# Kernel tuning notes

Hardware: AMD Instinct MI355X
Metric: run time of the kernel (lower is better)

## Reference

```python
import jax, jax.numpy as jnp
import numpy as np

B, H, L, D, BLK = 2, 16, 2048, 64, 32
NB = L // BLK          # 64 blocks per side
WINDOW = 8             # causal local window, in blocks


def make_layout():
    # [H, NB, NB] int32: block (i, j) active iff 0 <= i - j < WINDOW (causal local band)
    bi = jnp.arange(NB)
    band = ((bi[:, None] - bi[None, :]) >= 0) & ((bi[:, None] - bi[None, :]) < WINDOW)
    return jnp.broadcast_to(band[None].astype(jnp.int32), (H, NB, NB))


def setup_inputs() -> dict:
    rng = jax.random.key(0)
    kq, kk, kv, kp = jax.random.split(rng, 4)
    return {
        "query": jax.random.normal(kq, (B, H, L, D), dtype=jnp.float32),
        "key": jax.random.normal(kk, (B, H, L, D), dtype=jnp.float32),
        "value": jax.random.normal(kv, (B, H, L, D), dtype=jnp.float32),
        "key_padding_mask": jax.random.normal(kp, (B, L), dtype=jnp.float32),
        "layout": make_layout(),
    }


def reference(query, key, value, key_padding_mask, layout):
    # query/key/value: [B, H, L, D]; layout: [H, NB, NB] block sparsity pattern
    bsz, num_heads, tgt_len, head_dim = query.shape
    blk = tgt_len // layout.shape[1]
    scaling = float(head_dim) ** (-0.5)

    # SDD: scores only on active blocks. Reference computes dense then masks
    # inactive blocks to -inf, matching blocksparse softmax semantics exactly.
    scores = jnp.einsum("bhqd,bhkd->bhqk", query, key) * scaling
    # key_padding_mask_mode='add': added to logits, broadcast over queries
    scores = scores + key_padding_mask[:, None, None, :]

    # expand block layout [H, NB, NB] -> element mask [H, L, L]
    block_mask = jnp.repeat(jnp.repeat(layout.astype(bool), blk, axis=1), blk, axis=2)
    scores = jnp.where(block_mask[None], scores, -jnp.inf)

    probs = jax.nn.softmax(scores, axis=-1)  # zeros outside active blocks
    # DSD: probs @ value
    attn_output = jnp.einsum("bhqk,bhkd->bhqd", probs, value)
    return attn_output
```

## Files before the change

### kernel.cpp

```cpp
#include <hip/hip_runtime.h>

#define B_   2
#define H_   16
#define L_   2048
#define D_   64
#define BLK_ 32
#define NB_  64

#define KSW 64
#define VS  40
#define OS  65

typedef __bf16 bf16x8 __attribute__((ext_vector_type(8)));
typedef float  f32x4  __attribute__((ext_vector_type(4)));
typedef unsigned short u16x8 __attribute__((ext_vector_type(8)));

__device__ inline unsigned short f2bf(float f) {
    unsigned int u = __builtin_bit_cast(unsigned int, f);
    unsigned int r = u + 0x7fffu + ((u >> 16) & 1u);
    return (unsigned short)(r >> 16);
}
#define WG_BARRIER() asm volatile("s_waitcnt lgkmcnt(0)\n\ts_barrier" ::: "memory")

__global__ __launch_bounds__(128)
__attribute__((amdgpu_waves_per_eu(4, 4)))
void sparse_attn_kernel(const float* __restrict__ qg,
                        const float* __restrict__ kg,
                        const float* __restrict__ vg,
                        const float* __restrict__ kpm,
                        const int*   __restrict__ layout,
                        float* __restrict__ outg)
{
    __shared__ __align__(16) union {
        struct {
            unsigned short Ks[2][BLK_ * KSW];
            unsigned short Vt[2][D_ * VS];
        } s;
        float Os[32 * OS];
    } Lds;

    const int tid  = threadIdx.x;
    const int wave = tid >> 6;
    const int lane = tid & 63;
    const int quad = lane >> 4;
    const int l15  = lane & 15;

    const int phys = blockIdx.x;
    const int lw   = (phys & 7) * 256 + (phys >> 3);
    const int i = lw & 63;
    const int h = (lw >> 6) & 15;
    const int b = lw >> 10;

    const size_t bh = (size_t)(b * H_ + h);
    const float* kbase = kg + bh * L_ * D_;
    const float* vbase = vg + bh * L_ * D_;
    const float* kpp   = kpm + (size_t)b * L_;
    const int*   layrow = layout + (h * NB_ + i) * NB_;

    const int jbeg = i - 7;
    int act[8];
    #pragma unroll
    for (int s = 0; s < 8; ++s) {
        const int j = jbeg + s;
        act[s] = (j >= 0) ? layrow[j] : 0;
    }

    bf16x8 aq[2];
    {
        const float* qrow = qg + (bh * L_ + (size_t)i * BLK_ + wave * 16 + l15) * D_;
        #pragma unroll
        for (int ks = 0; ks < 2; ++ks) {
            float4 x = *(const float4*)&qrow[ks * 32 + quad * 8];
            float4 y = *(const float4*)&qrow[ks * 32 + quad * 8 + 4];
            u16x8 pk;
            pk[0]=f2bf(x.x); pk[1]=f2bf(x.y); pk[2]=f2bf(x.z); pk[3]=f2bf(x.w);
            pk[4]=f2bf(y.x); pk[5]=f2bf(y.y); pk[6]=f2bf(y.z); pk[7]=f2bf(y.w);
            aq[ks] = __builtin_bit_cast(bf16x8, pk);
        }
    }

    auto clampj = [&](int j) { return j < 0 ? 0 : j; };

    u16x8 kc[2][2];
    u16x8 vc[2][2];

    auto loadT = [&](int jc, int slot) {
        const float* kb = kbase + (size_t)jc * BLK_ * D_;
        float4 a0 = *(const float4*)&kb[tid * 8];
        float4 a1 = *(const float4*)&kb[tid * 8 + 4];
        float4 b0 = *(const float4*)&kb[(tid + 128) * 8];
        float4 b1 = *(const float4*)&kb[(tid + 128) * 8 + 4];
        u16x8 k0, k1;
        k0[0]=f2bf(a0.x); k0[1]=f2bf(a0.y); k0[2]=f2bf(a0.z); k0[3]=f2bf(a0.w);
        k0[4]=f2bf(a1.x); k0[5]=f2bf(a1.y); k0[6]=f2bf(a1.z); k0[7]=f2bf(a1.w);
        k1[0]=f2bf(b0.x); k1[1]=f2bf(b0.y); k1[2]=f2bf(b0.z); k1[3]=f2bf(b0.w);
        k1[4]=f2bf(b1.x); k1[5]=f2bf(b1.y); k1[6]=f2bf(b1.z); k1[7]=f2bf(b1.w);
        kc[slot][0] = k0; kc[slot][1] = k1;
        const float* vb = vbase + (size_t)jc * BLK_ * D_;
        #pragma unroll
        for (int cc = 0; cc < 2; ++cc) {
            u16x8 pv;
            #pragma unroll
            for (int r = 0; r < 4; ++r) {
                pv[r]     = f2bf(vb[(wave * 8 + cc * 4 + r) * D_ + lane]);
                pv[4 + r] = f2bf(vb[(16 + wave * 8 + cc * 4 + r) * D_ + lane]);
            }
            vc[slot][cc] = pv;
        }
    };

    auto storeT = [&](int buf, int slot) {
        const int row = tid >> 3, oct = tid & 7;
        *(u16x8*)&Lds.s.Ks[buf][row * KSW + ((oct ^ (row & 7)) * 8)]        = kc[slot][0];
        *(u16x8*)&Lds.s.Ks[buf][(16 + row) * KSW + ((oct ^ (row & 7)) * 8)] = kc[slot][1];
        const int swz = lane & 3;
        #pragma unroll
        for (int cc = 0; cc < 2; ++cc)
            *(u16x8*)&Lds.s.Vt[buf][lane * VS + (((2 * wave + cc) ^ swz) * 8)] = vc[slot][cc];
    };

    float lsum = 0.f;
    f32x4 Ot[4];
    #pragma unroll
    for (int t = 0; t < 4; ++t) Ot[t] = (f32x4){0.f, 0.f, 0.f, 0.f};

    auto computeT = [&](int buf, int j) {
        float4 kp0 = *(const float4*)&kpp[j * BLK_ + quad * 4];
        float4 kp1 = *(const float4*)&kpp[j * BLK_ + 16 + quad * 4];
        f32x4 st0 = {0.f,0.f,0.f,0.f}, st1 = {0.f,0.f,0.f,0.f};
        #pragma unroll
        for (int ks = 0; ks < 2; ++ks) {
            const int co = (((ks * 4 + quad) ^ (l15 & 7)) * 8);
            bf16x8 ka  = *(const bf16x8*)&Lds.s.Ks[buf][l15 * KSW + co];
            bf16x8 kb2 = *(const bf16x8*)&Lds.s.Ks[buf][(16 + l15) * KSW + co];
            st0 = __builtin_amdgcn_mfma_f32_16x16x32_bf16(ka,  aq[ks], st0, 0, 0, 0);
            st1 = __builtin_amdgcn_mfma_f32_16x16x32_bf16(kb2, aq[ks], st1, 0, 0, 0);
        }
        u16x8 bpk;
        #pragma unroll
        for (int r = 0; r < 4; ++r) {
            float p0 = __expf(st0[r] * 0.125f + kp0[r]);
            float p1 = __expf(st1[r] * 0.125f + kp1[r]);
            lsum += p0 + p1;
            bpk[r]     = f2bf(p0);
            bpk[4 + r] = f2bf(p1);
        }
        bf16x8 bp = __builtin_bit_cast(bf16x8, bpk);
        const int swzv = l15 & 3;
        #pragma unroll
        for (int t = 0; t < 4; ++t) {
            bf16x8 av = *(const bf16x8*)&Lds.s.Vt[buf][(t * 16 + l15) * VS + ((quad ^ swzv) * 8)];
            Ot[t] = __builtin_amdgcn_mfma_f32_16x16x32_bf16(av, bp, Ot[t], 0, 0, 0);
        }
    };

    loadT(clampj(jbeg), 0);
    storeT(0, 0);
    loadT(clampj(jbeg + 1), 1);
    WG_BARRIER();

    int cur = 0;
    #pragma unroll
    for (int s = 0; s < 8; ++s) {
        const int j = jbeg + s;
        if (s <= 5) loadT(clampj(j + 2), s & 1);
        if (act[s] != 0) computeT(cur, j);
        if (s < 7) storeT(cur ^ 1, (s + 1) & 1);
        WG_BARRIER();
        cur ^= 1;
    }

    lsum += __shfl_xor(lsum, 16);
    lsum += __shfl_xor(lsum, 32);
    const float rinv = 1.0f / lsum;

    float* osw = &Lds.Os[(wave * 16) * OS];
    #pragma unroll
    for (int t = 0; t < 4; ++t)
        #pragma unroll
        for (int r = 0; r < 4; ++r)
            osw[l15 * OS + t * 16 + quad * 4 + r] = Ot[t][r] * rinv;
    asm volatile("s_waitcnt lgkmcnt(0)" ::: "memory");

    const int qrow = lane >> 2, sc = lane & 3;
    float* outp = outg + (bh * L_ + (size_t)i * BLK_ + wave * 16) * D_;
    #pragma unroll
    for (int c = 0; c < 4; ++c) {
        float4 gv;
        #pragma unroll
        for (int r = 0; r < 4; ++r) gv[r] = osw[qrow * OS + c * 16 + sc * 4 + r];
        *(float4*)&outp[qrow * D_ + c * 16 + sc * 4] = gv;
    }
}

extern "C" void kernel_launch(void* const* d_in, const int* in_sizes, int n_in,
                              void* d_out, int out_size, void* d_ws, size_t ws_size,
                              hipStream_t stream) {
    const float* q      = (const float*)d_in[0];
    const float* k      = (const float*)d_in[1];
    const float* v      = (const float*)d_in[2];
    const float* kpmask = (const float*)d_in[3];
    const int*   layout = (const int*)d_in[4];
    float* out = (float*)d_out;

    dim3 grid(B_ * H_ * NB_);
    dim3 block(128);
    sparse_attn_kernel<<<grid, block, 0, stream>>>(q, k, v, kpmask, layout, out);
}
```

Before: 106.3 us.

## Precompute bf16 K and transposed V in a prep kernel, drop LDS staging

Adds a prep kernel that converts K to bf16 and V to a transposed bf16 layout in workspace once. The attention kernel then runs one wave per 16 query rows, loading MFMA operands straight from global memory with no LDS buffers or barriers, and writes the output directly from registers. This removes the eight-fold redundant fp32 loading and conversion of each K/V block across neighbouring query blocks and all barrier synchronisation. In exchange it adds a second launch, a workspace round trip, and global loads issued on the critical path without double-buffering.

```diff
diff --git a/kernel.cpp b/kernel.cpp
--- a/kernel.cpp
+++ b/kernel.cpp
@@ -6,10 +6,7 @@
 #define D_   64
 #define BLK_ 32
 #define NB_  64
-
-#define KSW 64
-#define VS  40
-#define OS  65
+#define BH_  (B_ * H_)
 
 typedef __bf16 bf16x8 __attribute__((ext_vector_type(8)));
 typedef float  f32x4  __attribute__((ext_vector_type(4)));
@@ -20,176 +17,144 @@
     unsigned int r = u + 0x7fffu + ((u >> 16) & 1u);
     return (unsigned short)(r >> 16);
 }
-#define WG_BARRIER() asm volatile("s_waitcnt lgkmcnt(0)\n\ts_barrier" ::: "memory")
+__device__ inline unsigned int pkt(float lo, float hi) {
+    return __builtin_amdgcn_perm(__builtin_bit_cast(unsigned int, hi),
+                                 __builtin_bit_cast(unsigned int, lo), 0x07060302u);
+}
 
-__global__ __launch_bounds__(128)
+__global__ __launch_bounds__(64)
+void prep_kernel(const float* __restrict__ kg, const float* __restrict__ vg,
+                 unsigned short* __restrict__ kbo, unsigned short* __restrict__ vto)
+{
+    const int lane = threadIdx.x;
+    const int wg = blockIdx.x;
+    const int j  = wg & (NB_ - 1);
+    const int bh = wg >> 6;
+
+    const float* ks = kg + ((size_t)bh * L_ + (size_t)j * BLK_) * D_;
+    unsigned short* kd = kbo + ((size_t)bh * L_ + (size_t)j * BLK_) * D_;
+    #pragma unroll
+    for (int e = 0; e < 4; ++e) {
+        float4 x = *(const float4*)&ks[lane * 32 + e * 8];
+        float4 y = *(const float4*)&ks[lane * 32 + e * 8 + 4];
+        u16x8 w;
+        w[0]=f2bf(x.x); w[1]=f2bf(x.y); w[2]=f2bf(x.z); w[3]=f2bf(x.w);
+        w[4]=f2bf(y.x); w[5]=f2bf(y.y); w[6]=f2bf(y.z); w[7]=f2bf(y.w);
+        *(u16x8*)&kd[lane * 32 + e * 8] = w;
+    }
+
+    const float* vs = vg + ((size_t)bh * L_ + (size_t)j * BLK_) * D_;
+    unsigned short* vd = vto + ((size_t)bh * D_ + lane) * L_ + (size_t)j * BLK_;
+    #pragma unroll
+    for (int e = 0; e < 4; ++e) {
+        u16x8 w;
+        #pragma unroll
+        for (int q = 0; q < 8; ++q) {
+            const int key = (q >> 2) * 16 + e * 4 + (q & 3);
+            w[q] = f2bf(vs[key * D_ + lane]);
+        }
+        *(u16x8*)&vd[e * 8] = w;
+    }
+}
+
+__global__ __launch_bounds__(64)
 __attribute__((amdgpu_waves_per_eu(4, 4)))
-void sparse_attn_kernel(const float* __restrict__ qg,
-                        const float* __restrict__ kg,
-                        const float* __restrict__ vg,
-                        const float* __restrict__ kpm,
-                        const int*   __restrict__ layout,
-                        float* __restrict__ outg)
+void attn_kernel(const float* __restrict__ qg,
+                 const float* __restrict__ kpm,
+                 const int*   __restrict__ layout,
+                 const unsigned short* __restrict__ kbi,
+                 const unsigned short* __restrict__ vti,
+                 float* __restrict__ outg)
 {
-    __shared__ __align__(16) union {
-        struct {
-            unsigned short Ks[2][BLK_ * KSW];
-            unsigned short Vt[2][D_ * VS];
-        } s;
-        float Os[32 * OS];
-    } Lds;
-
-    const int tid  = threadIdx.x;
-    const int wave = tid >> 6;
-    const int lane = tid & 63;
-    const int quad = lane >> 4;
-    const int l15  = lane & 15;
+    const int lane = threadIdx.x & 63;
+    const int quad = lane >> 4, l15 = lane & 15;
 
     const int phys = blockIdx.x;
-    const int lw   = (phys & 7) * 256 + (phys >> 3);
-    const int i = lw & 63;
-    const int h = (lw >> 6) & 15;
-    const int b = lw >> 10;
+    const int lw = (phys & 7) * 512 + (phys >> 3);
+    const int hf = lw & 1;
+    const int i  = (lw >> 1) & 63;
+    const int bh = lw >> 7;
+    const int b = bh >> 4, h = bh & 15;
 
-    const size_t bh = (size_t)(b * H_ + h);
-    const float* kbase = kg + bh * L_ * D_;
-    const float* vbase = vg + bh * L_ * D_;
-    const float* kpp   = kpm + (size_t)b * L_;
-    const int*   layrow = layout + (h * NB_ + i) * NB_;
+    const unsigned short* kbb = kbi + (size_t)bh * L_ * D_;
+    const unsigned short* vtb = vti + (size_t)bh * D_ * L_;
+    const float* kpp = kpm + (size_t)b * L_;
+    const int* layrow = layout + (h * NB_ + i) * NB_;
 
     const int jbeg = i - 7;
     int act[8];
     #pragma unroll
-    for (int s = 0; s < 8; ++s) {
-        const int j = jbeg + s;
-        act[s] = (j >= 0) ? layrow[j] : 0;
-    }
+    for (int s = 0; s < 8; ++s) { const int j = jbeg + s; act[s] = (j >= 0) ? layrow[j] : 0; }
 
     bf16x8 aq[2];
     {
-        const float* qrow = qg + (bh * L_ + (size_t)i * BLK_ + wave * 16 + l15) * D_;
+        const float* qrow = qg + ((size_t)bh * L_ + (size_t)i * BLK_ + hf * 16 + l15) * D_;
         #pragma unroll
         for (int ks = 0; ks < 2; ++ks) {
             float4 x = *(const float4*)&qrow[ks * 32 + quad * 8];
             float4 y = *(const float4*)&qrow[ks * 32 + quad * 8 + 4];
-            u16x8 pk;
-            pk[0]=f2bf(x.x); pk[1]=f2bf(x.y); pk[2]=f2bf(x.z); pk[3]=f2bf(x.w);
-            pk[4]=f2bf(y.x); pk[5]=f2bf(y.y); pk[6]=f2bf(y.z); pk[7]=f2bf(y.w);
-            aq[ks] = __builtin_bit_cast(bf16x8, pk);
+            uint4 p;
+            p.x = pkt(x.x, x.y); p.y = pkt(x.z, x.w);
+            p.z = pkt(y.x, y.y); p.w = pkt(y.z, y.w);
+            aq[ks] = __builtin_bit_cast(bf16x8, p);
         }
     }
-
-    auto clampj = [&](int j) { return j < 0 ? 0 : j; };
-
-    u16x8 kc[2][2];
-    u16x8 vc[2][2];
-
-    auto loadT = [&](int jc, int slot) {
-        const float* kb = kbase + (size_t)jc * BLK_ * D_;
-        float4 a0 = *(const float4*)&kb[tid * 8];
-        float4 a1 = *(const float4*)&kb[tid * 8 + 4];
-        float4 b0 = *(const float4*)&kb[(tid + 128) * 8];
-        float4 b1 = *(const float4*)&kb[(tid + 128) * 8 + 4];
-        u16x8 k0, k1;
-        k0[0]=f2bf(a0.x); k0[1]=f2bf(a0.y); k0[2]=f2bf(a0.z); k0[3]=f2bf(a0.w);
-        k0[4]=f2bf(a1.x); k0[5]=f2bf(a1.y); k0[6]=f2bf(a1.z); k0[7]=f2bf(a1.w);
-        k1[0]=f2bf(b0.x); k1[1]=f2bf(b0.y); k1[2]=f2bf(b0.z); k1[3]=f2bf(b0.w);
-        k1[4]=f2bf(b1.x); k1[5]=f2bf(b1.y); k1[6]=f2bf(b1.z); k1[7]=f2bf(b1.w);
-        kc[slot][0] = k0; kc[slot][1] = k1;
-        const float* vb = vbase + (size_t)jc * BLK_ * D_;
-        #pragma unroll
-        for (int cc = 0; cc < 2; ++cc) {
-            u16x8 pv;
-            #pragma unroll
-            for (int r = 0; r < 4; ++r) {
-                pv[r]     = f2bf(vb[(wave * 8 + cc * 4 + r) * D_ + lane]);
-                pv[4 + r] = f2bf(vb[(16 + wave * 8 + cc * 4 + r) * D_ + lane]);
-            }
-            vc[slot][cc] = pv;
-        }
-    };
-
-    auto storeT = [&](int buf, int slot) {
-        const int row = tid >> 3, oct = tid & 7;
-        *(u16x8*)&Lds.s.Ks[buf][row * KSW + ((oct ^ (row & 7)) * 8)]        = kc[slot][0];
-        *(u16x8*)&Lds.s.Ks[buf][(16 + row) * KSW + ((oct ^ (row & 7)) * 8)] = kc[slot][1];
-        const int swz = lane & 3;
-        #pragma unroll
-        for (int cc = 0; cc < 2; ++cc)
-            *(u16x8*)&Lds.s.Vt[buf][lane * VS + (((2 * wave + cc) ^ swz) * 8)] = vc[slot][cc];
-    };
 
     float lsum = 0.f;
     f32x4 Ot[4];
     #pragma unroll
     for (int t = 0; t < 4; ++t) Ot[t] = (f32x4){0.f, 0.f, 0.f, 0.f};
 
-    auto computeT = [&](int buf, int j) {
-        float4 kp0 = *(const float4*)&kpp[j * BLK_ + quad * 4];
-        float4 kp1 = *(const float4*)&kpp[j * BLK_ + 16 + quad * 4];
-        f32x4 st0 = {0.f,0.f,0.f,0.f}, st1 = {0.f,0.f,0.f,0.f};
-        #pragma unroll
-        for (int ks = 0; ks < 2; ++ks) {
-            const int co = (((ks * 4 + quad) ^ (l15 & 7)) * 8);
-            bf16x8 ka  = *(const bf16x8*)&Lds.s.Ks[buf][l15 * KSW + co];
-            bf16x8 kb2 = *(const bf16x8*)&Lds.s.Ks[buf][(16 + l15) * KSW + co];
-            st0 = __builtin_amdgcn_mfma_f32_16x16x32_bf16(ka,  aq[ks], st0, 0, 0, 0);
-            st1 = __builtin_amdgcn_mfma_f32_16x16x32_bf16(kb2, aq[ks], st1, 0, 0, 0);
-        }
-        u16x8 bpk;
-        #pragma unroll
-        for (int r = 0; r < 4; ++r) {
-            float p0 = __expf(st0[r] * 0.125f + kp0[r]);
-            float p1 = __expf(st1[r] * 0.125f + kp1[r]);
-            lsum += p0 + p1;
-            bpk[r]     = f2bf(p0);
-            bpk[4 + r] = f2bf(p1);
-        }
-        bf16x8 bp = __builtin_bit_cast(bf16x8, bpk);
-        const int swzv = l15 & 3;
-        #pragma unroll
-        for (int t = 0; t < 4; ++t) {
-            bf16x8 av = *(const bf16x8*)&Lds.s.Vt[buf][(t * 16 + l15) * VS + ((quad ^ swzv) * 8)];
-            Ot[t] = __builtin_amdgcn_mfma_f32_16x16x32_bf16(av, bp, Ot[t], 0, 0, 0);
-        }
-    };
-
-    loadT(clampj(jbeg), 0);
-    storeT(0, 0);
-    loadT(clampj(jbeg + 1), 1);
-    WG_BARRIER();
-
-    int cur = 0;
     #pragma unroll
     for (int s = 0; s < 8; ++s) {
-        const int j = jbeg + s;
-        if (s <= 5) loadT(clampj(j + 2), s & 1);
-        if (act[s] != 0) computeT(cur, j);
-        if (s < 7) storeT(cur ^ 1, (s + 1) & 1);
-        WG_BARRIER();
-        cur ^= 1;
+        const int j  = jbeg + s;
+        const int jc = j < 0 ? 0 : j;
+        const unsigned short* kt = kbb + (size_t)jc * BLK_ * D_;
+        bf16x8 k00 = *(const bf16x8*)&kt[l15 * D_ + quad * 8];
+        bf16x8 k01 = *(const bf16x8*)&kt[l15 * D_ + 32 + quad * 8];
+        bf16x8 k10 = *(const bf16x8*)&kt[(16 + l15) * D_ + quad * 8];
+        bf16x8 k11 = *(const bf16x8*)&kt[(16 + l15) * D_ + 32 + quad * 8];
+        bf16x8 av0 = *(const bf16x8*)&vtb[(size_t)(0 * 16 + l15) * L_ + jc * BLK_ + quad * 8];
+        bf16x8 av1 = *(const bf16x8*)&vtb[(size_t)(1 * 16 + l15) * L_ + jc * BLK_ + quad * 8];
+        bf16x8 av2 = *(const bf16x8*)&vtb[(size_t)(2 * 16 + l15) * L_ + jc * BLK_ + quad * 8];
+        bf16x8 av3 = *(const bf16x8*)&vtb[(size_t)(3 * 16 + l15) * L_ + jc * BLK_ + quad * 8];
+        float4 kp0 = *(const float4*)&kpp[jc * BLK_ + quad * 4];
+        float4 kp1 = *(const float4*)&kpp[jc * BLK_ + 16 + quad * 4];
+
+        if (act[s] != 0) {
+            f32x4 st0 = {0.f,0.f,0.f,0.f}, st1 = {0.f,0.f,0.f,0.f};
+            st0 = __builtin_amdgcn_mfma_f32_16x16x32_bf16(k00, aq[0], st0, 0, 0, 0);
+            st0 = __builtin_amdgcn_mfma_f32_16x16x32_bf16(k01, aq[1], st0, 0, 0, 0);
+            st1 = __builtin_amdgcn_mfma_f32_16x16x32_bf16(k10, aq[0], st1, 0, 0, 0);
+            st1 = __builtin_amdgcn_mfma_f32_16x16x32_bf16(k11, aq[1], st1, 0, 0, 0);
+            float p0[4], p1[4];
+            #pragma unroll
+            for (int r = 0; r < 4; ++r) {
+                p0[r] = __expf(st0[r] * 0.125f + kp0[r]);
+                p1[r] = __expf(st1[r] * 0.125f + kp1[r]);
+                lsum += p0[r] + p1[r];
+            }
+            uint4 pw;
+            pw.x = pkt(p0[0], p0[1]); pw.y = pkt(p0[2], p0[3]);
+            pw.z = pkt(p1[0], p1[1]); pw.w = pkt(p1[2], p1[3]);
+            bf16x8 bp = __builtin_bit_cast(bf16x8, pw);
+            Ot[0] = __builtin_amdgcn_mfma_f32_16x16x32_bf16(av0, bp, Ot[0], 0, 0, 0);
+            Ot[1] = __builtin_amdgcn_mfma_f32_16x16x32_bf16(av1, bp, Ot[1], 0, 0, 0);
+            Ot[2] = __builtin_amdgcn_mfma_f32_16x16x32_bf16(av2, bp, Ot[2], 0, 0, 0);
+            Ot[3] = __builtin_amdgcn_mfma_f32_16x16x32_bf16(av3, bp, Ot[3], 0, 0, 0);
+        }
     }
 
     lsum += __shfl_xor(lsum, 16);
     lsum += __shfl_xor(lsum, 32);
     const float rinv = 1.0f / lsum;
-
-    float* osw = &Lds.Os[(wave * 16) * OS];
+    float* outp = outg + ((size_t)bh * L_ + (size_t)i * BLK_ + hf * 16 + l15) * D_;
     #pragma unroll
-    for (int t = 0; t < 4; ++t)
-        #pragma unroll
-        for (int r = 0; r < 4; ++r)
-            osw[l15 * OS + t * 16 + quad * 4 + r] = Ot[t][r] * rinv;
-    asm volatile("s_waitcnt lgkmcnt(0)" ::: "memory");
-
-    const int qrow = lane >> 2, sc = lane & 3;
-    float* outp = outg + (bh * L_ + (size_t)i * BLK_ + wave * 16) * D_;
-    #pragma unroll
-    for (int c = 0; c < 4; ++c) {
-        float4 gv;
-        #pragma unroll
-        for (int r = 0; r < 4; ++r) gv[r] = osw[qrow * OS + c * 16 + sc * 4 + r];
-        *(float4*)&outp[qrow * D_ + c * 16 + sc * 4] = gv;
+    for (int t = 0; t < 4; ++t) {
+        float4 g;
+        g.x = Ot[t][0] * rinv; g.y = Ot[t][1] * rinv;
+        g.z = Ot[t][2] * rinv; g.w = Ot[t][3] * rinv;
+        *(float4*)&outp[t * 16 + quad * 4] = g;
     }
 }
 
@@ -203,7 +168,9 @@
     const int*   layout = (const int*)d_in[4];
     float* out = (float*)d_out;
 
-    dim3 grid(B_ * H_ * NB_);
-    dim3 block(128);
-    sparse_attn_kernel<<<grid, block, 0, stream>>>(q, k, v, kpmask, layout, out);
+    unsigned short* kb = (unsigned short*)d_ws;
+    unsigned short* vt = kb + (size_t)BH_ * L_ * D_;
+
+    prep_kernel<<<dim3(BH_ * NB_), dim3(64), 0, stream>>>(k, v, kb, vt);
+    attn_kernel<<<dim3(BH_ * NB_ * 2), dim3(64), 0, stream>>>(q, kpmask, layout, kb, vt, out);
 }
```

New measurement: 133.7 us. +25.8%, slower.
